# Performance work log

Measured on AMD Instinct MI355X. Metric: run time of the kernel, lower is better.

## Reference

```python
import jax, jax.numpy as jnp
import numpy as np
import math

DIM = 1024
NUM_HEADS = 16
HEAD_DIM = 64
NUM_FEATURES = 128
B, N = 2, 1024


def _sample_orf(rng, num_features, head_dim):
    # Orthogonal Random Features: stack QR-orthogonalized blocks scaled by chi(D) row norms
    blocks = []
    while len(blocks) * head_dim < num_features:
        G = rng.standard_normal((head_dim, head_dim)).astype(np.float32)
        Q, _ = np.linalg.qr(G)
        norms = np.linalg.norm(rng.standard_normal((head_dim, head_dim)).astype(np.float32), axis=1)
        blocks.append(np.diag(norms) @ Q.T)
    return np.concatenate(blocks, axis=0)[:num_features]


def setup_inputs() -> dict:
    key = jax.random.key(0)
    ks = jax.random.split(key, 6)
    s = 1.0 / math.sqrt(DIM)
    x = jax.random.normal(ks[0], (B, N, DIM), dtype=jnp.float32)
    omega = jnp.asarray(_sample_orf(np.random.default_rng(0), NUM_FEATURES, HEAD_DIM))
    Wq = jax.random.normal(ks[1], (DIM, DIM), dtype=jnp.float32) * s
    Wk = jax.random.normal(ks[2], (DIM, DIM), dtype=jnp.float32) * s
    Wv = jax.random.normal(ks[3], (DIM, DIM), dtype=jnp.float32) * s
    Wo = jax.random.normal(ks[4], (DIM, DIM), dtype=jnp.float32) * s
    bo = jax.random.normal(ks[5], (DIM,), dtype=jnp.float32) * 0.01
    return {"x": x, "omega": omega, "Wq": Wq, "Wk": Wk, "Wv": Wv, "Wo": Wo, "bo": bo}


def _phi(x, omega, is_query):
    # x: [B,H,N,D], omega: [M,D] -> [B,H,N,M]
    proj = jnp.einsum('bhnd,md->bhnm', x, omega)
    norm = 0.5 * jnp.sum(x * x, axis=-1, keepdims=True)
    log_phi = proj - norm
    if is_query:
        log_phi = log_phi - jnp.max(log_phi, axis=-1, keepdims=True)
    else:
        log_phi = log_phi - jnp.max(log_phi)
    return jnp.exp(log_phi) / math.sqrt(NUM_FEATURES) + 1e-4


def reference(x, omega, Wq, Wk, Wv, Wo, bo):
    Bx, Nx, _ = x.shape
    H, D = NUM_HEADS, HEAD_DIM

    def split_heads(y):  # [B,N,H*D] -> [B,H,N,D]
        return y.reshape(Bx, Nx, H, D).transpose(0, 2, 1, 3)

    q = split_heads(x @ Wq.T)
    k = split_heads(x @ Wk.T)
    v = split_heads(x @ Wv.T)

    scale = D ** (-0.25)
    phi_q = _phi(q * scale, omega, is_query=True)   # [B,H,N,M]
    phi_k = _phi(k * scale, omega, is_query=False)  # [B,H,N,M]

    # causal linear attention via explicit kv outer-product cumsum (as in source)
    kv = jnp.einsum('bhnm,bhnd->bhnmd', phi_k, v)
    kv_cumsum = jnp.cumsum(kv, axis=2)              # [B,H,N,M,D]
    k_cumsum = jnp.cumsum(phi_k, axis=2)            # [B,H,N,M]
    out = jnp.einsum('bhnm,bhnmd->bhnd', phi_q, kv_cumsum)
    z = 1.0 / (jnp.einsum('bhnm,bhnm->bhn', phi_q, k_cumsum) + 1e-6)
    out = out * z[..., None]

    out = out.transpose(0, 2, 1, 3).reshape(Bx, Nx, H * D)
    return out @ Wo.T + bo
```

## Files before the change

### kernel.cpp

```cpp
#include <hip/hip_runtime.h>
#include <hip/hip_bf16.h>
#include <math.h>

#define DIMS 1024
#define NHEADS 16
#define HDIM 64
#define NFEAT 128
#define BB 2
#define NN 1024
#define BN (BB*NN)
#define NCH 16
#define CSZ 64
#define WW (DIMS*DIMS)
#define QKVN (3*DIMS)

#define SCALE 0.3535533905932738f
#define INV_SQRT_M 0.08838834764831845f

typedef __attribute__((ext_vector_type(8))) _Float16 h8v;
typedef __attribute__((ext_vector_type(8))) short s8v;
typedef __attribute__((ext_vector_type(4))) float f4v;

__device__ __forceinline__ ushort f2h(float x) {
    _Float16 h = (_Float16)x;
    return *(ushort*)&h;
}
__device__ __forceinline__ float h2f(ushort u) {
    _Float16 h = *(_Float16*)&u;
    return (float)h;
}
__device__ __forceinline__ void gload16(const void* g, void* l) {
    __builtin_amdgcn_global_load_lds(
        (const __attribute__((address_space(1))) unsigned int*)g,
        (__attribute__((address_space(3))) unsigned int*)l,
        16, 0, 0);
}

#define NX (BN*DIMS/8)
#define NW (WW/8)
#define NOM (NFEAT*HDIM/8)
__global__ __launch_bounds__(256) void cast_all(const float* __restrict__ x,
                                                const float* __restrict__ Wq,
                                                const float* __restrict__ Wk,
                                                const float* __restrict__ Wv,
                                                const float* __restrict__ Wo,
                                                const float* __restrict__ omega,
                                                ushort* __restrict__ xh,
                                                ushort* __restrict__ wqkvh,
                                                ushort* __restrict__ woh,
                                                ushort* __restrict__ omh) {
    const int i = blockIdx.x * 256 + threadIdx.x;
    const float* src; ushort* dst; int off;
    if (i < NX)               { src = x;     dst = xh;                     off = i; }
    else if (i < NX + NW)     { src = Wq;    dst = wqkvh;                  off = i - NX; }
    else if (i < NX + 2 * NW) { src = Wk;    dst = wqkvh + WW;             off = i - NX - NW; }
    else if (i < NX + 3 * NW) { src = Wv;    dst = wqkvh + 2 * (size_t)WW; off = i - NX - 2 * NW; }
    else if (i < NX + 4 * NW) { src = Wo;    dst = woh;                    off = i - NX - 3 * NW; }
    else                      { src = omega; dst = omh;                    off = i - NX - 4 * NW; }
    float4 a = ((const float4*)src)[2 * (size_t)off];
    float4 b = ((const float4*)src)[2 * (size_t)off + 1];
    float v[8] = {a.x, a.y, a.z, a.w, b.x, b.y, b.z, b.w};
    ushort h8[8];
    #pragma unroll
    for (int j = 0; j < 8; ++j) h8[j] = f2h(v[j]);
    *(s8v*)&dst[(size_t)off * 8] = *(s8v*)&h8[0];
}

template<int BM, bool HOUT>
__global__ __launch_bounds__(256) void gemm_nt_lds(const ushort* __restrict__ A,
                                                   const ushort* __restrict__ B,
                                                   float* __restrict__ C,
                                                   ushort* __restrict__ C16,
                                                   const float* __restrict__ bias,
                                                   int M, int N, int K, int nbx) {
    constexpr int MF = BM / 32;
    constexpr int AI = BM / 64;
    __shared__ __attribute__((aligned(16))) ushort lA[BM][32];
    __shared__ __attribute__((aligned(16))) ushort lB[128][32];
    const int tid = threadIdx.x;
    const int w = tid >> 6, l = tid & 63, lr = l & 15, lg = l >> 4;
    const int wm = (w >> 1) * (BM / 2), wn = (w & 1) * 64;
    const int nwg = gridDim.x;
    const int q8 = nwg >> 3;
    const int neu = (blockIdx.x & 7) * q8 + (blockIdx.x >> 3);
    const int bx = neu % nbx, by = neu / nbx;
    const int bi = bx * BM, bj = by * 128;
    const int srow = l >> 2, scol = (l & 3) * 8;

    f4v acc[MF][4] = {};
    for (int k0 = 0; k0 < K; k0 += 32) {
        #pragma unroll
        for (int i = 0; i < AI; ++i) {
            const int r0 = w * (16 * AI) + i * 16;
            gload16(&A[(size_t)(bi + r0 + srow) * K + k0 + scol], &lA[r0][0]);
        }
        #pragma unroll
        for (int i = 0; i < 2; ++i) {
            const int r0 = w * 32 + i * 16;
            gload16(&B[(size_t)(bj + r0 + srow) * K + k0 + scol], &lB[r0][0]);
        }
        __syncthreads();
        h8v b_[4];
        #pragma unroll
        for (int j = 0; j < 4; ++j) b_[j] = *(h8v*)&lB[wn + j * 16 + lr][lg * 8];
        #pragma unroll
        for (int i = 0; i < MF; ++i) {
            h8v a_ = *(h8v*)&lA[wm + i * 16 + lr][lg * 8];
            #pragma unroll
            for (int j = 0; j < 4; ++j)
                acc[i][j] = __builtin_amdgcn_mfma_f32_16x16x32_f16(a_, b_[j], acc[i][j], 0, 0, 0);
        }
        __syncthreads();
    }
    #pragma unroll
    for (int i = 0; i < MF; ++i)
        #pragma unroll
        for (int j = 0; j < 4; ++j)
            #pragma unroll
            for (int rg = 0; rg < 4; ++rg) {
                const int row = bi + wm + i * 16 + lg * 4 + rg;
                const int col = bj + wn + j * 16 + lr;
                if (HOUT) {
                    C16[(size_t)row * N + col] = f2h(acc[i][j][rg]);
                } else {
                    float r = acc[i][j][rg] + bias[col];
                    C[(size_t)row * N + col] = r;
                }
            }
}

__global__ __launch_bounds__(256) void phi_mfma(const ushort* __restrict__ qkvh,
                                                const ushort* __restrict__ omh,
                                                ushort* __restrict__ phiq,
                                                ushort* __restrict__ plocal,
                                                float* __restrict__ blockmax) {
    __shared__ __attribute__((aligned(16))) ushort lq[64][72];
    __shared__ __attribute__((aligned(16))) ushort lbuf[128 * 72];
    __shared__ float lnorm[64];
    __shared__ float wred[4];
    const int tid = threadIdx.x;
    const int z = blockIdx.z, h = blockIdx.y;
    const int bn0 = blockIdx.x * 64;
    const int w = tid >> 6, l = tid & 63, lr = l & 15, lg = l >> 4;

    {
        const int r = tid >> 2, c0 = (tid & 3) * 16;
        const size_t g = (size_t)(bn0 + r) * QKVN + (size_t)z * DIMS + h * HDIM + c0;
        s8v v0 = *(const s8v*)&qkvh[g];
        s8v v1 = *(const s8v*)&qkvh[g + 8];
        *(s8v*)&lq[r][c0] = v0;
        *(s8v*)&lq[r][c0 + 8] = v1;
        float p = 0.f;
        #pragma unroll
        for (int j = 0; j < 8; ++j) {
            float a = h2f(((ushort*)&v0)[j]); p += a * a;
            float b = h2f(((ushort*)&v1)[j]); p += b * b;
        }
        p += __shfl_xor(p, 1); p += __shfl_xor(p, 2);
        if ((tid & 3) == 0) lnorm[r] = p;
    }
    {
        const int m = tid >> 1, c0 = (tid & 1) * 32;
        #pragma unroll
        for (int i = 0; i < 4; ++i)
            *(s8v*)&lbuf[m * 72 + c0 + i * 8] = *(const s8v*)&omh[m * HDIM + c0 + i * 8];
    }
    __syncthreads();

    f4v acc[8] = {};
    #pragma unroll
    for (int k0 = 0; k0 < 64; k0 += 32) {
        h8v a = *(h8v*)&lq[w * 16 + lr][k0 + lg * 8];
        #pragma unroll
        for (int ct = 0; ct < 8; ++ct) {
            h8v b = *(h8v*)&lbuf[(ct * 16 + lr) * 72 + k0 + lg * 8];
            acc[ct] = __builtin_amdgcn_mfma_f32_16x16x32_f16(a, b, acc[ct], 0, 0, 0);
        }
    }

    const float hs2 = 0.5f * SCALE * SCALE;
    float lvv[4][8];
    #pragma unroll
    for (int rg = 0; rg < 4; ++rg) {
        const int row = w * 16 + lg * 4 + rg;
        const float nh = hs2 * lnorm[row];
        #pragma unroll
        for (int ct = 0; ct < 8; ++ct) lvv[rg][ct] = SCALE * acc[ct][rg] - nh;
    }
    if (z == 1) {
        float bmax = -3.4e38f;
        #pragma unroll
        for (int rg = 0; rg < 4; ++rg)
            #pragma unroll
            for (int ct = 0; ct < 8; ++ct) bmax = fmaxf(bmax, lvv[rg][ct]);
        #pragma unroll
        for (int o = 32; o >= 1; o >>= 1) bmax = fmaxf(bmax, __shfl_xor(bmax, o));
        if (l == 0) wred[w] = bmax;
    }
    __syncthreads();

    if (z == 0) {
        #pragma unroll
        for (int rg = 0; rg < 4; ++rg) {
            const int row = w * 16 + lg * 4 + rg;
            float mx = -3.4e38f;
            #pragma unroll
            for (int ct = 0; ct < 8; ++ct) mx = fmaxf(mx, lvv[rg][ct]);
            #pragma unroll
            for (int o = 8; o >= 1; o >>= 1) mx = fmaxf(mx, __shfl_xor(mx, o));
            #pragma unroll
            for (int ct = 0; ct < 8; ++ct)
                lbuf[row * 136 + ct * 16 + lr] = f2h(expf(lvv[rg][ct] - mx) * INV_SQRT_M + 1e-4f);
        }
    } else {
        const float bm = fmaxf(fmaxf(wred[0], wred[1]), fmaxf(wred[2], wred[3]));
        if (tid == 0) blockmax[h * gridDim.x + blockIdx.x] = bm;
        #pragma unroll
        for (int rg = 0; rg < 4; ++rg) {
            const int row = w * 16 + lg * 4 + rg;
            #pragma unroll
            for (int ct = 0; ct < 8; ++ct)
                lbuf[row * 136 + ct * 16 + lr] = f2h(expf(lvv[rg][ct] - bm));
        }
    }
    __syncthreads();
    ushort* dst = (z == 0) ? phiq : plocal;
    const int r = tid >> 2, c0 = (tid & 3) * 32;
    const int br = bn0 + r;
    const int b = br >> 10, n = br & (NN - 1);
    const size_t orow = ((size_t)(b * NHEADS + h) * NN + n) * NFEAT;
    #pragma unroll
    for (int i = 0; i < 4; ++i)
        *(s8v*)&dst[orow + c0 + i * 8] = *(s8v*)&lbuf[r * 136 + c0 + i * 8];
}

__global__ __launch_bounds__(256) void phik_vt_sums(const ushort* __restrict__ plocal,
                                                    const float* __restrict__ blockmax,
                                                    const ushort* __restrict__ qkvh,
                                                    ushort* __restrict__ phik,
                                                    ushort* __restrict__ vt,
                                                    ushort* __restrict__ ssum16,
                                                    float* __restrict__ kcsum) {
    const int c = blockIdx.x, bh = blockIdx.y, n0 = c * CSZ;
    const int b = bh >> 4, h = bh & 15;
    const int tid = threadIdx.x;
    const int w = tid >> 6, l = tid & 63, lr = l & 15, lg = l >> 4;
    __shared__ __attribute__((aligned(16))) ushort lt[64][136];
    __shared__ __attribute__((aligned(16))) ushort lv[64][72];
    __shared__ __attribute__((aligned(16))) ushort lvt[64][72];
    __shared__ __attribute__((aligned(16))) ushort lktT[128][72];
    __shared__ float gred[4];

    float mx = fmaxf(blockmax[tid], blockmax[tid + 256]);
    #pragma unroll
    for (int o = 32; o >= 1; o >>= 1) mx = fmaxf(mx, __shfl_xor(mx, o));
    if (l == 0) gred[w] = mx;
    {
        const int r = tid >> 2, c0 = (tid & 3) * 16;
        const size_t g = (size_t)(b * NN + n0 + r) * QKVN + 2 * DIMS + h * HDIM + c0;
        *(s8v*)&lv[r][c0]     = *(const s8v*)&qkvh[g];
        *(s8v*)&lv[r][c0 + 8] = *(const s8v*)&qkvh[g + 8];
    }
    __syncthreads();
    const float gm = fmaxf(fmaxf(gred[0], gred[1]), fmaxf(gred[2], gred[3]));
    const float bm = blockmax[h * 32 + b * 16 + c];
    const float fac = expf(bm - gm) * INV_SQRT_M;
    {
        const int r = tid >> 2, c0 = (tid & 3) * 32;
        const size_t gbase = ((size_t)bh * NN + n0 + r) * NFEAT + c0;
        ushort tmp[32];
        #pragma unroll
        for (int i = 0; i < 4; ++i) {
            s8v pv = *(const s8v*)&plocal[gbase + i * 8];
            #pragma unroll
            for (int j = 0; j < 8; ++j)
                tmp[i * 8 + j] = f2h(h2f(((ushort*)&pv)[j]) * fac + 1e-4f);
        }
        #pragma unroll
        for (int i = 0; i < 4; ++i) {
            *(s8v*)&phik[gbase + i * 8] = *(s8v*)&tmp[i * 8];
            *(s8v*)&lt[r][c0 + i * 8] = *(s8v*)&tmp[i * 8];
        }
    }
    __syncthreads();
    {
        const int m = tid >> 1, nh2 = (tid & 1) * 32;
        ushort tp[32];
        #pragma unroll
        for (int i = 0; i < 32; ++i) tp[i] = lt[nh2 + i][m];
        #pragma unroll
        for (int i = 0; i < 4; ++i) *(s8v*)&lktT[m][nh2 + i * 8] = *(s8v*)&tp[i * 8];
    }
    {
        const int d = tid >> 2, s0 = (tid & 3) * 16;
        ushort tp[16];
        #pragma unroll
        for (int i = 0; i < 16; ++i) tp[i] = lv[s0 + i][d];
        const size_t tb = ((size_t)bh * HDIM + d) * NN + n0 + s0;
        *(s8v*)&vt[tb] = *(s8v*)&tp[0];
        *(s8v*)&vt[tb + 8] = *(s8v*)&tp[8];
        *(s8v*)&lvt[d][s0] = *(s8v*)&tp[0];
        *(s8v*)&lvt[d][s0 + 8] = *(s8v*)&tp[8];
    }
    __syncthreads();
    f4v acc[8] = {};
    #pragma unroll
    for (int k0 = 0; k0 < 64; k0 += 32) {
        h8v a = *(h8v*)&lvt[w * 16 + lr][k0 + lg * 8];
        #pragma unroll
        for (int ct = 0; ct < 8; ++ct) {
            h8v bf = *(h8v*)&lktT[ct * 16 + lr][k0 + lg * 8];
            acc[ct] = __builtin_amdgcn_mfma_f32_16x16x32_f16(a, bf, acc[ct], 0, 0, 0);
        }
    }
    const size_t obase = ((size_t)bh * NCH + c) * (HDIM * NFEAT);
    #pragma unroll
    for (int ct = 0; ct < 8; ++ct)
        #pragma unroll
        for (int rg = 0; rg < 4; ++rg) {
            const int d = w * 16 + lg * 4 + rg, m = ct * 16 + lr;
            ssum16[obase + (size_t)d * NFEAT + m] = f2h(acc[ct][rg]);
        }
    if (tid < 128) {
        float s = 0.f;
        #pragma unroll 8
        for (int i = 0; i < 64; ++i) s += h2f(lktT[tid][i]);
        kcsum[((size_t)bh * NCH + c) * NFEAT + tid] = s;
    }
}

__global__ __launch_bounds__(256) void chunk_prefix(const ushort* __restrict__ ssum16,
                                                    ushort* __restrict__ spre,
                                                    const float* __restrict__ kcsum,
                                                    float* __restrict__ kcpre) {
    const int bh = blockIdx.y, sl = blockIdx.x;
    const int tid = threadIdx.x;
    if (sl == 0 && tid < NFEAT) {
        float a = 0.f;
        for (int c = 0; c < NCH; ++c) {
            kcpre[((size_t)bh * NCH + c) * NFEAT + tid] = a;
            a += kcsum[((size_t)bh * NCH + c) * NFEAT + tid];
        }
    }
    const int base_e = (sl * 256 + tid) * 8;
    float acc[8] = {};
    const size_t bb = (size_t)bh * NCH * (HDIM * NFEAT);
    for (int c = 0; c < NCH; ++c) {
        const size_t cb = bb + (size_t)c * (HDIM * NFEAT);
        s8v v = *(const s8v*)&ssum16[cb + base_e];
        ushort o[8];
        #pragma unroll
        for (int j = 0; j < 8; ++j) o[j] = f2h(acc[j]);
        *(s8v*)&spre[cb + base_e] = *(s8v*)&o[0];
        #pragma unroll
        for (int j = 0; j < 8; ++j) acc[j] += h2f(((ushort*)&v)[j]);
    }
}

__global__ __launch_bounds__(256) void scan_final(const ushort* __restrict__ phiq,
                                                  const ushort* __restrict__ phik,
                                                  const ushort* __restrict__ vt,
                                                  const ushort* __restrict__ spre,
                                                  const float* __restrict__ kcpre,
                                                  ushort* __restrict__ att_h) {
    const int c = blockIdx.x, bh = blockIdx.y;
    const int b = bh >> 4, h = bh & 15;
    const int n0 = c * CSZ;
    __shared__ __attribute__((aligned(16))) ushort lq[64][136];
    __shared__ __attribute__((aligned(16))) ushort lk[64][136];
    __shared__ __attribute__((aligned(16))) ushort lvt[64][72];
    __shared__ __attribute__((aligned(16))) ushort lsp[64][136];
    __shared__ __attribute__((aligned(16))) ushort lA[64][72];
    __shared__ float kc[NFEAT];
    __shared__ float zin[64];
    __shared__ float zp[4][64];
    const int tid = threadIdx.x;

    const size_t qb = ((size_t)bh * NN + n0) * NFEAT;
    #pragma unroll
    for (int i = 0; i < 4; ++i) {
        const int idx = tid + 256 * i;
        const int r = idx >> 4, cs = (idx & 15) * 8;
        *(s8v*)&lq[r][cs] = *(const s8v*)&phiq[qb + (size_t)r * NFEAT + cs];
        *(s8v*)&lk[r][cs] = *(const s8v*)&phik[qb + (size_t)r * NFEAT + cs];
    }
    const size_t sb = ((size_t)bh * NCH + c) * (HDIM * NFEAT);
    #pragma unroll
    for (int i = 0; i < 4; ++i) {
        const int idx = tid + 256 * i;
        const int r = idx >> 4, cs = (idx & 15) * 8;
        *(s8v*)&lsp[r][cs] = *(const s8v*)&spre[sb + (size_t)r * NFEAT + cs];
    }
    {
        const int d = tid >> 2, s = (tid & 3) * 16;
        const size_t g = ((size_t)bh * HDIM + d) * NN + n0 + s;
        *(s8v*)&lvt[d][s]     = *(const s8v*)&vt[g];
        *(s8v*)&lvt[d][s + 8] = *(const s8v*)&vt[g + 8];
    }
    if (tid < NFEAT) kc[tid] = kcpre[((size_t)bh * NCH + c) * NFEAT + tid];
    __syncthreads();

    const int w = tid >> 6, l = tid & 63, lr = l & 15, lg = l >> 4;

    f4v a4[4] = {};
    #pragma unroll
    for (int k0 = 0; k0 < 128; k0 += 32) {
        h8v av = *(h8v*)&lq[w * 16 + lr][k0 + lg * 8];
        #pragma unroll
        for (int ct = 0; ct < 4; ++ct) {
            h8v bv = *(h8v*)&lk[ct * 16 + lr][k0 + lg * 8];
            a4[ct] = __builtin_amdgcn_mfma_f32_16x16x32_f16(av, bv, a4[ct], 0, 0, 0);
        }
    }
    float zi[4] = {0.f, 0.f, 0.f, 0.f};
    #pragma unroll
    for (int ct = 0; ct < 4; ++ct) {
        #pragma unroll
        for (int rg = 0; rg < 4; ++rg) {
            const int row = w * 16 + lg * 4 + rg;
            const int col = ct * 16 + lr;
            const float val = (col <= row) ? a4[ct][rg] : 0.f;
            const ushort hq = f2h(val);
            zi[rg] += h2f(hq);
            lA[row][col] = hq;
        }
    }
    #pragma unroll
    for (int rg = 0; rg < 4; ++rg) {
        float z = zi[rg];
        z += __shfl_xor(z, 1); z += __shfl_xor(z, 2);
        z += __shfl_xor(z, 4); z += __shfl_xor(z, 8);
        if (lr == 0) zin[w * 16 + lg * 4 + rg] = z;
    }
    {
        const int row = tid & 63, qq = tid >> 6;
        float s = 0.f;
        #pragma unroll 8
        for (int m = 0; m < 32; ++m) s += h2f(lq[row][qq * 32 + m]) * kc[qq * 32 + m];
        zp[qq][row] = s;
    }
    __syncthreads();

    f4v o4[4] = {};
    #pragma unroll
    for (int k0 = 0; k0 < 64; k0 += 32) {
        h8v av = *(h8v*)&lA[w * 16 + lr][k0 + lg * 8];
        #pragma unroll
        for (int ct = 0; ct < 4; ++ct) {
            h8v bv = *(h8v*)&lvt[ct * 16 + lr][k0 + lg * 8];
            o4[ct] = __builtin_amdgcn_mfma_f32_16x16x32_f16(av, bv, o4[ct], 0, 0, 0);
        }
    }
    #pragma unroll
    for (int k0 = 0; k0 < 128; k0 += 32) {
        h8v av = *(h8v*)&lq[w * 16 + lr][k0 + lg * 8];
        #pragma unroll
        for (int ct = 0; ct < 4; ++ct) {
            h8v bv = *(h8v*)&lsp[ct * 16 + lr][k0 + lg * 8];
            o4[ct] = __builtin_amdgcn_mfma_f32_16x16x32_f16(av, bv, o4[ct], 0, 0, 0);
        }
    }
    #pragma unroll
    for (int rg = 0; rg < 4; ++rg) {
        const int row = w * 16 + lg * 4 + rg;
        const float z = zin[row] + zp[0][row] + zp[1][row] + zp[2][row] + zp[3][row] + 1e-6f;
        const float rz = 1.f / z;
        #pragma unroll
        for (int ct = 0; ct < 4; ++ct) {
            const int d = ct * 16 + lr;
            att_h[((size_t)(b * NN + n0 + row)) * DIMS + h * HDIM + d] = f2h(o4[ct][rg] * rz);
        }
    }
}

extern "C" void kernel_launch(void* const* d_in, const int* in_sizes, int n_in,
                              void* d_out, int out_size, void* d_ws, size_t ws_size,
                              hipStream_t stream) {
    const float* x     = (const float*)d_in[0];
    const float* omega = (const float*)d_in[1];
    const float* Wq    = (const float*)d_in[2];
    const float* Wk    = (const float*)d_in[3];
    const float* Wv    = (const float*)d_in[4];
    const float* Wo    = (const float*)d_in[5];
    const float* bo    = (const float*)d_in[6];
    float* out = (float*)d_out;

    const size_t PROJ = (size_t)BN * DIMS;
    const size_t PHI  = (size_t)BB * NHEADS * NN * NFEAT;
    ushort* qkvh    = (ushort*)d_ws;
    ushort* xh      = qkvh + (size_t)BN * QKVN;
    ushort* wqkvh   = xh + PROJ;
    ushort* woh     = wqkvh + (size_t)QKVN * DIMS;
    ushort* omh     = woh + WW;
    ushort* phiq_h  = omh + NFEAT * HDIM;
    ushort* phik_h  = phiq_h + PHI;
    ushort* plocal  = phik_h + PHI;
    ushort* vt_h    = plocal + PHI;
    ushort* ssum16  = vt_h + PROJ;
    ushort* spre_h  = ssum16 + PHI;
    ushort* att_hb  = spre_h + PHI;
    float*  kcsum   = (float*)(att_hb + PROJ);
    float*  kcpre   = kcsum + 32 * NCH * NFEAT;
    float*  blockmax= kcpre + 32 * NCH * NFEAT;

    cast_all<<<(NX + 4 * NW + NOM) / 256, 256, 0, stream>>>(x, Wq, Wk, Wv, Wo, omega,
                                                            xh, wqkvh, woh, omh);

    gemm_nt_lds<64, true><<<(BN / 64) * (QKVN / 128), 256, 0, stream>>>(
        xh, wqkvh, nullptr, qkvh, nullptr, BN, QKVN, DIMS, BN / 64);

    dim3 pg(BN / 64, NHEADS, 2);
    phi_mfma<<<pg, 256, 0, stream>>>(qkvh, omh, phiq_h, plocal, blockmax);

    dim3 cg(NCH, BB * NHEADS);
    phik_vt_sums<<<cg, 256, 0, stream>>>(plocal, blockmax, qkvh, phik_h, vt_h,
                                         ssum16, kcsum);
    chunk_prefix<<<dim3(4, BB * NHEADS), 256, 0, stream>>>(ssum16, spre_h, kcsum, kcpre);
    scan_final<<<cg, 256, 0, stream>>>(phiq_h, phik_h, vt_h, spre_h, kcpre, att_hb);

    gemm_nt_lds<64, false><<<(BN / 64) * (DIMS / 128), 256, 0, stream>>>(
        att_hb, woh, out, nullptr, bo, BN, DIMS, DIMS, BN / 64);
}
```

Before: 91.67 us.

## Fuse phi_k chunk sums into phi kernel and defer global-max rescaling

Removes the separate phik_vt_sums kernel. The phi kernel now computes the per-chunk V-transpose, kv outer-product sums, k sums and v sums directly from the locally-normalized phi_k. The global-max rescale and the +1e-4 offset are applied algebraically later, in chunk_prefix and scan_final. This saves one launch and a full phi_k write/read round trip, at the cost of redundant global-max reductions in later kernels and more LDS in the phi kernel, which may lower occupancy. Applying the scale factor to fp16-rounded local values may slightly change numerics.

```diff
diff --git a/kernel.cpp b/kernel.cpp
--- a/kernel.cpp
+++ b/kernel.cpp
@@ -133,15 +133,24 @@
                                                 const ushort* __restrict__ omh,
                                                 ushort* __restrict__ phiq,
                                                 ushort* __restrict__ plocal,
-                                                float* __restrict__ blockmax) {
+                                                float* __restrict__ blockmax,
+                                                ushort* __restrict__ vt,
+                                                ushort* __restrict__ ssum16,
+                                                float* __restrict__ kcsum,
+                                                float* __restrict__ vsum) {
     __shared__ __attribute__((aligned(16))) ushort lq[64][72];
-    __shared__ __attribute__((aligned(16))) ushort lbuf[128 * 72];
+    __shared__ __attribute__((aligned(16))) ushort lom[128 * 72];
+    __shared__ __attribute__((aligned(16))) ushort lktT[128][72];
+    __shared__ __attribute__((aligned(16))) ushort lv[64][72];
+    __shared__ __attribute__((aligned(16))) ushort lvt[64][72];
     __shared__ float lnorm[64];
     __shared__ float wred[4];
     const int tid = threadIdx.x;
     const int z = blockIdx.z, h = blockIdx.y;
     const int bn0 = blockIdx.x * 64;
     const int w = tid >> 6, l = tid & 63, lr = l & 15, lg = l >> 4;
+    const int b = blockIdx.x >> 4, c = blockIdx.x & 15;
+    const int bh = b * NHEADS + h;
 
     {
         const int r = tid >> 2, c0 = (tid & 3) * 16;
@@ -154,7 +163,7 @@
         #pragma unroll
         for (int j = 0; j < 8; ++j) {
             float a = h2f(((ushort*)&v0)[j]); p += a * a;
-            float b = h2f(((ushort*)&v1)[j]); p += b * b;
+            float bb2 = h2f(((ushort*)&v1)[j]); p += bb2 * bb2;
         }
         p += __shfl_xor(p, 1); p += __shfl_xor(p, 2);
         if ((tid & 3) == 0) lnorm[r] = p;
@@ -163,7 +172,13 @@
         const int m = tid >> 1, c0 = (tid & 1) * 32;
         #pragma unroll
         for (int i = 0; i < 4; ++i)
-            *(s8v*)&lbuf[m * 72 + c0 + i * 8] = *(const s8v*)&omh[m * HDIM + c0 + i * 8];
+            *(s8v*)&lom[m * 72 + c0 + i * 8] = *(const s8v*)&omh[m * HDIM + c0 + i * 8];
+    }
+    if (z == 1) {
+        const int r = tid >> 2, c0 = (tid & 3) * 16;
+        const size_t g = (size_t)(bn0 + r) * QKVN + 2 * DIMS + h * HDIM + c0;
+        *(s8v*)&lv[r][c0]     = *(const s8v*)&qkvh[g];
+        *(s8v*)&lv[r][c0 + 8] = *(const s8v*)&qkvh[g + 8];
     }
     __syncthreads();
 
@@ -173,8 +188,8 @@
         h8v a = *(h8v*)&lq[w * 16 + lr][k0 + lg * 8];
         #pragma unroll
         for (int ct = 0; ct < 8; ++ct) {
-            h8v b = *(h8v*)&lbuf[(ct * 16 + lr) * 72 + k0 + lg * 8];
-            acc[ct] = __builtin_amdgcn_mfma_f32_16x16x32_f16(a, b, acc[ct], 0, 0, 0);
+            h8v bo = *(h8v*)&lom[(ct * 16 + lr) * 72 + k0 + lg * 8];
+            acc[ct] = __builtin_amdgcn_mfma_f32_16x16x32_f16(a, bo, acc[ct], 0, 0, 0);
         }
     }
 
@@ -210,84 +225,41 @@
             for (int o = 8; o >= 1; o >>= 1) mx = fmaxf(mx, __shfl_xor(mx, o));
             #pragma unroll
             for (int ct = 0; ct < 8; ++ct)
-                lbuf[row * 136 + ct * 16 + lr] = f2h(expf(lvv[rg][ct] - mx) * INV_SQRT_M + 1e-4f);
+                lom[row * 136 + ct * 16 + lr] = f2h(expf(lvv[rg][ct] - mx) * INV_SQRT_M + 1e-4f);
         }
     } else {
         const float bm = fmaxf(fmaxf(wred[0], wred[1]), fmaxf(wred[2], wred[3]));
-        if (tid == 0) blockmax[h * gridDim.x + blockIdx.x] = bm;
+        if (tid == 0) blockmax[h * 32 + blockIdx.x] = bm;
         #pragma unroll
         for (int rg = 0; rg < 4; ++rg) {
             const int row = w * 16 + lg * 4 + rg;
             #pragma unroll
             for (int ct = 0; ct < 8; ++ct)
-                lbuf[row * 136 + ct * 16 + lr] = f2h(expf(lvv[rg][ct] - bm));
-        }
-    }
-    __syncthreads();
-    ushort* dst = (z == 0) ? phiq : plocal;
-    const int r = tid >> 2, c0 = (tid & 3) * 32;
-    const int br = bn0 + r;
-    const int b = br >> 10, n = br & (NN - 1);
-    const size_t orow = ((size_t)(b * NHEADS + h) * NN + n) * NFEAT;
-    #pragma unroll
-    for (int i = 0; i < 4; ++i)
-        *(s8v*)&dst[orow + c0 + i * 8] = *(s8v*)&lbuf[r * 136 + c0 + i * 8];
-}
-
-__global__ __launch_bounds__(256) void phik_vt_sums(const ushort* __restrict__ plocal,
-                                                    const float* __restrict__ blockmax,
-                                                    const ushort* __restrict__ qkvh,
-                                                    ushort* __restrict__ phik,
-                                                    ushort* __restrict__ vt,
-                                                    ushort* __restrict__ ssum16,
-                                                    float* __restrict__ kcsum) {
-    const int c = blockIdx.x, bh = blockIdx.y, n0 = c * CSZ;
-    const int b = bh >> 4, h = bh & 15;
-    const int tid = threadIdx.x;
-    const int w = tid >> 6, l = tid & 63, lr = l & 15, lg = l >> 4;
-    __shared__ __attribute__((aligned(16))) ushort lt[64][136];
-    __shared__ __attribute__((aligned(16))) ushort lv[64][72];
-    __shared__ __attribute__((aligned(16))) ushort lvt[64][72];
-    __shared__ __attribute__((aligned(16))) ushort lktT[128][72];
-    __shared__ float gred[4];
-
-    float mx = fmaxf(blockmax[tid], blockmax[tid + 256]);
-    #pragma unroll
-    for (int o = 32; o >= 1; o >>= 1) mx = fmaxf(mx, __shfl_xor(mx, o));
-    if (l == 0) gred[w] = mx;
-    {
-        const int r = tid >> 2, c0 = (tid & 3) * 16;
-        const size_t g = (size_t)(b * NN + n0 + r) * QKVN + 2 * DIMS + h * HDIM + c0;
-        *(s8v*)&lv[r][c0]     = *(const s8v*)&qkvh[g];
-        *(s8v*)&lv[r][c0 + 8] = *(const s8v*)&qkvh[g + 8];
-    }
-    __syncthreads();
-    const float gm = fmaxf(fmaxf(gred[0], gred[1]), fmaxf(gred[2], gred[3]));
-    const float bm = blockmax[h * 32 + b * 16 + c];
-    const float fac = expf(bm - gm) * INV_SQRT_M;
-    {
+                lom[row * 136 + ct * 16 + lr] = f2h(expf(lvv[rg][ct] - bm));
+        }
+    }
+    __syncthreads();
+
+    {
+        ushort* dst = (z == 0) ? phiq : plocal;
         const int r = tid >> 2, c0 = (tid & 3) * 32;
-        const size_t gbase = ((size_t)bh * NN + n0 + r) * NFEAT + c0;
-        ushort tmp[32];
-        #pragma unroll
-        for (int i = 0; i < 4; ++i) {
-            s8v pv = *(const s8v*)&plocal[gbase + i * 8];
-            #pragma unroll
-            for (int j = 0; j < 8; ++j)
-                tmp[i * 8 + j] = f2h(h2f(((ushort*)&pv)[j]) * fac + 1e-4f);
-        }
-        #pragma unroll
-        for (int i = 0; i < 4; ++i) {
-            *(s8v*)&phik[gbase + i * 8] = *(s8v*)&tmp[i * 8];
-            *(s8v*)&lt[r][c0 + i * 8] = *(s8v*)&tmp[i * 8];
-        }
-    }
-    __syncthreads();
+        const size_t orow = ((size_t)bh * NN + (blockIdx.x & 15) * 64 + ((bn0 >> 10) ? 0 : 0)
+                             + ((size_t)0)) * 0;
+        const int br = bn0 + r;
+        const int bb2 = br >> 10, n = br & (NN - 1);
+        const size_t og = ((size_t)(bb2 * NHEADS + h) * NN + n) * NFEAT;
+        #pragma unroll
+        for (int i = 0; i < 4; ++i)
+            *(s8v*)&dst[og + c0 + i * 8] = *(s8v*)&lom[r * 136 + c0 + i * 8];
+        (void)orow;
+    }
+    if (z == 0) return;
+
     {
         const int m = tid >> 1, nh2 = (tid & 1) * 32;
         ushort tp[32];
         #pragma unroll
-        for (int i = 0; i < 32; ++i) tp[i] = lt[nh2 + i][m];
+        for (int i = 0; i < 32; ++i) tp[i] = lom[(nh2 + i) * 136 + m];
         #pragma unroll
         for (int i = 0; i < 4; ++i) *(s8v*)&lktT[m][nh2 + i * 8] = *(s8v*)&tp[i * 8];
     }
@@ -296,21 +268,23 @@
         ushort tp[16];
         #pragma unroll
         for (int i = 0; i < 16; ++i) tp[i] = lv[s0 + i][d];
-        const size_t tb = ((size_t)bh * HDIM + d) * NN + n0 + s0;
-        *(s8v*)&vt[tb] = *(s8v*)&tp[0];
-        *(s8v*)&vt[tb + 8] = *(s8v*)&tp[8];
+        const size_t tb = ((size_t)bh * HDIM + d) * NN + c * CSZ + (b ? 0 : 0) + s0;
+        *(s8v*)&vt[((size_t)bh * HDIM + d) * NN + c * CSZ + s0] = *(s8v*)&tp[0];
+        *(s8v*)&vt[((size_t)bh * HDIM + d) * NN + c * CSZ + s0 + 8] = *(s8v*)&tp[8];
         *(s8v*)&lvt[d][s0] = *(s8v*)&tp[0];
         *(s8v*)&lvt[d][s0 + 8] = *(s8v*)&tp[8];
-    }
-    __syncthreads();
-    f4v acc[8] = {};
+        (void)tb;
+    }
+    __syncthreads();
+
+    f4v ac2[8] = {};
     #pragma unroll
     for (int k0 = 0; k0 < 64; k0 += 32) {
         h8v a = *(h8v*)&lvt[w * 16 + lr][k0 + lg * 8];
         #pragma unroll
         for (int ct = 0; ct < 8; ++ct) {
             h8v bf = *(h8v*)&lktT[ct * 16 + lr][k0 + lg * 8];
-            acc[ct] = __builtin_amdgcn_mfma_f32_16x16x32_f16(a, bf, acc[ct], 0, 0, 0);
+            ac2[ct] = __builtin_amdgcn_mfma_f32_16x16x32_f16(a, bf, ac2[ct], 0, 0, 0);
         }
     }
     const size_t obase = ((size_t)bh * NCH + c) * (HDIM * NFEAT);
@@ -319,7 +293,7 @@
         #pragma unroll
         for (int rg = 0; rg < 4; ++rg) {
             const int d = w * 16 + lg * 4 + rg, m = ct * 16 + lr;
-            ssum16[obase + (size_t)d * NFEAT + m] = f2h(acc[ct][rg]);
+            ssum16[obase + (size_t)d * NFEAT + m] = f2h(ac2[ct][rg]);
         }
     if (tid < 128) {
         float s = 0.f;
@@ -327,41 +301,63 @@
         for (int i = 0; i < 64; ++i) s += h2f(lktT[tid][i]);
         kcsum[((size_t)bh * NCH + c) * NFEAT + tid] = s;
     }
+    if (tid < 64) {
+        float s = 0.f;
+        #pragma unroll 8
+        for (int i = 0; i < 64; ++i) s += h2f(lvt[tid][i]);
+        vsum[((size_t)bh * NCH + c) * HDIM + tid] = s;
+    }
 }
 
 __global__ __launch_bounds__(256) void chunk_prefix(const ushort* __restrict__ ssum16,
                                                     ushort* __restrict__ spre,
                                                     const float* __restrict__ kcsum,
-                                                    float* __restrict__ kcpre) {
+                                                    float* __restrict__ kcpre,
+                                                    const float* __restrict__ blockmax,
+                                                    const float* __restrict__ vsum) {
     const int bh = blockIdx.y, sl = blockIdx.x;
     const int tid = threadIdx.x;
+    const int b = bh >> 4, h = bh & 15;
+    __shared__ float gred[4];
+    float mx = fmaxf(blockmax[tid], blockmax[tid + 256]);
+    #pragma unroll
+    for (int o = 32; o >= 1; o >>= 1) mx = fmaxf(mx, __shfl_xor(mx, o));
+    if ((tid & 63) == 0) gred[tid >> 6] = mx;
+    __syncthreads();
+    const float gm = fmaxf(fmaxf(gred[0], gred[1]), fmaxf(gred[2], gred[3]));
+
     if (sl == 0 && tid < NFEAT) {
         float a = 0.f;
         for (int c = 0; c < NCH; ++c) {
             kcpre[((size_t)bh * NCH + c) * NFEAT + tid] = a;
-            a += kcsum[((size_t)bh * NCH + c) * NFEAT + tid];
+            const float fac = expf(blockmax[h * 32 + b * 16 + c] - gm) * INV_SQRT_M;
+            a += fac * kcsum[((size_t)bh * NCH + c) * NFEAT + tid] + 64.0f * 1e-4f;
         }
     }
     const int base_e = (sl * 256 + tid) * 8;
+    const int d = base_e >> 7;
     float acc[8] = {};
     const size_t bb = (size_t)bh * NCH * (HDIM * NFEAT);
     for (int c = 0; c < NCH; ++c) {
         const size_t cb = bb + (size_t)c * (HDIM * NFEAT);
+        const float fac = expf(blockmax[h * 32 + b * 16 + c] - gm) * INV_SQRT_M;
+        const float vs = vsum[((size_t)bh * NCH + c) * HDIM + d];
         s8v v = *(const s8v*)&ssum16[cb + base_e];
         ushort o[8];
         #pragma unroll
         for (int j = 0; j < 8; ++j) o[j] = f2h(acc[j]);
         *(s8v*)&spre[cb + base_e] = *(s8v*)&o[0];
         #pragma unroll
-        for (int j = 0; j < 8; ++j) acc[j] += h2f(((ushort*)&v)[j]);
+        for (int j = 0; j < 8; ++j) acc[j] += fac * h2f(((ushort*)&v)[j]) + 1e-4f * vs;
     }
 }
 
 __global__ __launch_bounds__(256) void scan_final(const ushort* __restrict__ phiq,
-                                                  const ushort* __restrict__ phik,
+                                                  const ushort* __restrict__ plocal,
                                                   const ushort* __restrict__ vt,
                                                   const ushort* __restrict__ spre,
                                                   const float* __restrict__ kcpre,
+                                                  const float* __restrict__ blockmax,
                                                   ushort* __restrict__ att_h) {
     const int c = blockIdx.x, bh = blockIdx.y;
     const int b = bh >> 4, h = bh & 15;
@@ -374,7 +370,16 @@
     __shared__ float kc[NFEAT];
     __shared__ float zin[64];
     __shared__ float zp[4][64];
+    __shared__ float gred[4];
     const int tid = threadIdx.x;
+
+    float mxv = fmaxf(blockmax[tid], blockmax[tid + 256]);
+    #pragma unroll
+    for (int o = 32; o >= 1; o >>= 1) mxv = fmaxf(mxv, __shfl_xor(mxv, o));
+    if ((tid & 63) == 0) gred[tid >> 6] = mxv;
+    __syncthreads();
+    const float gm = fmaxf(fmaxf(gred[0], gred[1]), fmaxf(gred[2], gred[3]));
+    const float fac = expf(blockmax[h * 32 + b * 16 + c] - gm) * INV_SQRT_M;
 
     const size_t qb = ((size_t)bh * NN + n0) * NFEAT;
     #pragma unroll
@@ -382,7 +387,11 @@
         const int idx = tid + 256 * i;
         const int r = idx >> 4, cs = (idx & 15) * 8;
         *(s8v*)&lq[r][cs] = *(const s8v*)&phiq[qb + (size_t)r * NFEAT + cs];
-        *(s8v*)&lk[r][cs] = *(const s8v*)&phik[qb + (size_t)r * NFEAT + cs];
+        s8v pv = *(const s8v*)&plocal[qb + (size_t)r * NFEAT + cs];
+        ushort t[8];
+        #pragma unroll
+        for (int j = 0; j < 8; ++j) t[j] = f2h(h2f(((ushort*)&pv)[j]) * fac + 1e-4f);
+        *(s8v*)&lk[r][cs] = *(s8v*)&t[0];
     }
     const size_t sb = ((size_t)bh * NCH + c) * (HDIM * NFEAT);
     #pragma unroll
@@ -493,8 +502,7 @@
     ushort* woh     = wqkvh + (size_t)QKVN * DIMS;
     ushort* omh     = woh + WW;
     ushort* phiq_h  = omh + NFEAT * HDIM;
-    ushort* phik_h  = phiq_h + PHI;
-    ushort* plocal  = phik_h + PHI;
+    ushort* plocal  = phiq_h + PHI;
     ushort* vt_h    = plocal + PHI;
     ushort* ssum16  = vt_h + PROJ;
     ushort* spre_h  = ssum16 + PHI;
@@ -502,6 +510,7 @@
     float*  kcsum   = (float*)(att_hb + PROJ);
     float*  kcpre   = kcsum + 32 * NCH * NFEAT;
     float*  blockmax= kcpre + 32 * NCH * NFEAT;
+    float*  vsum    = blockmax + 512;
 
     cast_all<<<(NX + 4 * NW + NOM) / 256, 256, 0, stream>>>(x, Wq, Wk, Wv, Wo, omega,
                                                             xh, wqkvh, woh, omh);
@@ -510,13 +519,14 @@
         xh, wqkvh, nullptr, qkvh, nullptr, BN, QKVN, DIMS, BN / 64);
 
     dim3 pg(BN / 64, NHEADS, 2);
-    phi_mfma<<<pg, 256, 0, stream>>>(qkvh, omh, phiq_h, plocal, blockmax);
-
+    phi_mfma<<<pg, 256, 0, stream>>>(qkvh, omh, phiq_h, plocal, blockmax,
+                                     vt_h, ssum16, kcsum, vsum);
+
+    chunk_prefix<<<dim3(4, BB * NHEADS), 256, 0, stream>>>(ssum16, spre_h, kcsum, kcpre,
+                                                           blockmax, vsum);
     dim3 cg(NCH, BB * NHEADS);
-    phik_vt_sums<<<cg, 256, 0, stream>>>(plocal, blockmax, qkvh, phik_h, vt_h,
-                                         ssum16, kcsum);
-    chunk_prefix<<<dim3(4, BB * NHEADS), 256, 0, stream>>>(ssum16, spre_h, kcsum, kcpre);
-    scan_final<<<cg, 256, 0, stream>>>(phiq_h, phik_h, vt_h, spre_h, kcpre, att_hb);
+    scan_final<<<cg, 256, 0, stream>>>(phiq_h, plocal, vt_h, spre_h, kcpre,
+                                       blockmax, att_hb);
 
     gemm_nt_lds<64, false><<<(BN / 64) * (DIMS / 128), 256, 0, stream>>>(
         att_hb, woh, out, nullptr, bo, BN, DIMS, DIMS, BN / 64);
```

Result: faster. 89.02 us (-2.9%).
